# Performance work log

Measured on AMD Instinct MI355X. Metric: run time of the kernel, lower is better.

The kernel has to match this reference:

```python
import jax, jax.numpy as jnp
import numpy as np

N_TOKEN = 267735
D_EMBED = 1024
D_PROJ = 1024
CUTOFF_ENDS = [0, 20000, 40000, 200000, N_TOKEN]
DIV_VAL = 4
INIT_STD = 0.02


def setup_inputs() -> dict:
    key = jax.random.key(0)
    ks = jax.random.split(key, 9)
    inp = jax.random.randint(ks[0], (8, 4096), 0, N_TOKEN, dtype=jnp.int64)
    out = {"inp": inp}
    for i in range(4):
        l, r = CUTOFF_ENDS[i], CUTOFF_ENDS[i + 1]
        d_emb_i = D_EMBED // (DIV_VAL ** i)
        out[f"emb{i}"] = jax.random.normal(ks[1 + i], (r - l, d_emb_i), dtype=jnp.float32) * INIT_STD
        out[f"proj{i}"] = jax.random.normal(ks[5 + i], (d_emb_i, D_PROJ), dtype=jnp.float32) * INIT_STD
    return out


def reference(inp, emb0, emb1, emb2, emb3, proj0, proj1, proj2, proj3):
    embs = [emb0, emb1, emb2, emb3]
    projs = [proj0, proj1, proj2, proj3]
    flat = inp.reshape(-1)  # [N]
    out = jnp.zeros((flat.shape[0], D_PROJ), dtype=jnp.float32)
    for i in range(4):
        l, r = CUTOFF_ENDS[i], CUTOFF_ENDS[i + 1]
        mask = (flat >= l) & (flat < r)  # [N]
        idx = jnp.clip(flat - l, 0, r - l - 1)  # in-range even for out-of-bucket tokens
        e = embs[i][idx]                         # [N, d_emb_i] gather
        p = jnp.einsum('id,de->ie', e, projs[i])  # [N, D_PROJ]
        out = out + jnp.where(mask[:, None], p, 0.0)
    emb_scale = D_PROJ ** 0.5
    return (out * emb_scale).reshape(inp.shape + (D_PROJ,))
```

## Files before the change

### kernel.cpp

```cpp
#include <hip/hip_runtime.h>
#include <hip/hip_bf16.h>

#define N_TOK   32768
#define DPROJ   1024
#define SCALE   32.0f

typedef short bf16x8 __attribute__((ext_vector_type(8)));
typedef float f32x4  __attribute__((ext_vector_type(4)));

__device__ __forceinline__ short f2bf(float f) {
    unsigned u = __builtin_bit_cast(unsigned, f);
    unsigned r = (u + 0x7FFFu + ((u >> 16) & 1u)) >> 16;
    return (short)r;
}

__global__ void k_prep(const int* __restrict__ inp, int* __restrict__ cnt,
                       int* __restrict__ perm, int* __restrict__ rowidx,
                       const float* __restrict__ p0, const float* __restrict__ p1,
                       const float* __restrict__ p2, const float* __restrict__ p3,
                       short* __restrict__ t0, short* __restrict__ t1,
                       short* __restrict__ t2, short* __restrict__ t3)
{
    __shared__ float tile[128][17];

    if (blockIdx.x < 128) {
        int i = blockIdx.x * 256 + threadIdx.x;
        int t = inp[i];
        int b, l;
        if (t < 20000)       { b = 0; l = 0; }
        else if (t < 40000)  { b = 1; l = 20000; }
        else if (t < 200000) { b = 2; l = 40000; }
        else                 { b = 3; l = 200000; }

        unsigned long long m0 = __ballot(b == 0);
        unsigned long long m1 = __ballot(b == 1);
        unsigned long long m2 = __ballot(b == 2);
        unsigned long long m3 = __ballot(b == 3);

        int lane = threadIdx.x & 63;
        int mybase = 0;
        if (lane < 4) {
            unsigned long long mm = (lane == 0) ? m0 : (lane == 1) ? m1 : (lane == 2) ? m2 : m3;
            mybase = atomicAdd(&cnt[lane], __popcll(mm));
        }
        int base = __shfl(mybase, b);
        unsigned long long mine = (b == 0) ? m0 : (b == 1) ? m1 : (b == 2) ? m2 : m3;
        unsigned long long lt = (lane == 0) ? 0ull : (~0ull >> (64 - lane));
        int pos = base + __popcll(mine & lt);
        perm[b * N_TOK + pos]   = i;
        rowidx[b * N_TOK + pos] = t - l;
        return;
    }

    int bid = blockIdx.x - 128;
    const float* src; short* dst; int K; int rel;
    if (bid < 512)      { src = p0; dst = t0; K = 1024; rel = bid; }
    else if (bid < 640) { src = p1; dst = t1; K = 256;  rel = bid - 512; }
    else if (bid < 704) { src = p2; dst = t2; K = 64;   rel = bid - 640; }
    else                { src = p3; dst = t3; K = 16;   rel = bid - 704; }
    int ktiles = (K + 127) >> 7;
    int k0 = (rel % ktiles) * 128;
    int n0 = (rel / ktiles) * 16;
    int t = threadIdx.x;

    #pragma unroll
    for (int i = 0; i < 2; ++i) {
        int idx = t + i * 256;
        int k = idx >> 2;
        int nc = (idx & 3) * 4;
        if (k0 + k < K) {
            float4 v = *reinterpret_cast<const float4*>(src + (size_t)(k0 + k) * DPROJ + n0 + nc);
            tile[k][nc + 0] = v.x; tile[k][nc + 1] = v.y;
            tile[k][nc + 2] = v.z; tile[k][nc + 3] = v.w;
        }
    }
    __syncthreads();
    int n  = t >> 4;
    int kc = (t & 15) * 8;
    if (k0 + kc < K) {
        short s[8];
        #pragma unroll
        for (int j = 0; j < 8; ++j) s[j] = f2bf(tile[kc + j][n]);
        *reinterpret_cast<int4*>(dst + (size_t)(n0 + n) * K + k0 + kc) =
            *reinterpret_cast<const int4*>(s);
    }
}

__global__ __launch_bounds__(512, 4) void k_gemm(
    const float* __restrict__ e0, const float* __restrict__ e1,
    const float* __restrict__ e2, const float* __restrict__ e3,
    const short* __restrict__ t0, const short* __restrict__ t1,
    const short* __restrict__ t2, const short* __restrict__ t3,
    const int* __restrict__ cnt, const int* __restrict__ perm,
    const int* __restrict__ rowidx, float* __restrict__ out)
{
    __shared__ short As[64][40];
    __shared__ short Bs[256][40];

    const int hw     = blockIdx.y * 4 + blockIdx.x;
    const int ytile  = (hw >> 5) * 8 + (hw & 7);
    const int panel  = (hw >> 3) & 3;

    const int c0 = cnt[0], c1 = cnt[1], c2 = cnt[2], c3 = cnt[3];
    const int q0 = (c0 + 63) & ~63;
    const int q1 = q0 + ((c1 + 63) & ~63);
    const int q2 = q1 + ((c2 + 63) & ~63);
    const int q3 = q2 + ((c3 + 63) & ~63);
    const int p0 = ytile * 64;
    if (p0 >= q3) return;
    int b, M, m0, K; const float* emb; const short* bt;
    if (p0 < q0)      { b = 0; M = c0; m0 = p0;      K = 1024; emb = e0; bt = t0; }
    else if (p0 < q1) { b = 1; M = c1; m0 = p0 - q0; K = 256;  emb = e1; bt = t1; }
    else if (p0 < q2) { b = 2; M = c2; m0 = p0 - q1; K = 64;   emb = e2; bt = t2; }
    else              { b = 3; M = c3; m0 = p0 - q2; K = 16;   emb = e3; bt = t3; }
    if (m0 >= M) return;
    const int* pperm = perm   + b * N_TOK;
    const int* prow  = rowidx + b * N_TOK;

    const int tid  = threadIdx.x;
    const int lane = tid & 63;
    const int w    = tid >> 6;
    const int n0   = panel * 256;

    const int ar = tid >> 3;
    const int ac4 = (tid & 7) * 4;
    const bool avalid = (m0 + ar) < M;
    const int  arow   = avalid ? prow[m0 + ar] : 0;
    const float* aptr = emb + (size_t)arow * K;
    const int br = tid >> 1;
    const int bh = (tid & 1) * 16;

    f32x4 acc[4][2];
    #pragma unroll
    for (int mi = 0; mi < 4; ++mi)
        #pragma unroll
        for (int ni = 0; ni < 2; ++ni) acc[mi][ni] = (f32x4)0.0f;

    const int koff = (lane >> 4) * 8;
    const int fr   = lane & 15;

    float4 av;
    int4   bv0, bv1;
#define ISSUE_LOADS(K0)                                                        \
    {                                                                          \
        av = make_float4(0.f, 0.f, 0.f, 0.f);                                  \
        if (avalid && ((K0) + ac4) < K)                                        \
            av = *reinterpret_cast<const float4*>(aptr + (K0) + ac4);          \
        if (((K0) + bh) < K) {                                                 \
            const short* bp = bt + (size_t)(n0 + br) * K + (K0) + bh;          \
            bv0 = *reinterpret_cast<const int4*>(bp);                          \
            bv1 = *reinterpret_cast<const int4*>(bp + 8);                      \
        } else {                                                               \
            bv0 = make_int4(0, 0, 0, 0);                                       \
            bv1 = make_int4(0, 0, 0, 0);                                       \
        }                                                                      \
    }

    ISSUE_LOADS(0);
    for (int k0 = 0; k0 < K; k0 += 32) {
        __syncthreads();
        {
            short asv[4];
            asv[0] = f2bf(av.x); asv[1] = f2bf(av.y);
            asv[2] = f2bf(av.z); asv[3] = f2bf(av.w);
            *reinterpret_cast<int2*>(&As[ar][ac4]) = *reinterpret_cast<const int2*>(asv);
            *reinterpret_cast<int4*>(&Bs[br][bh])     = bv0;
            *reinterpret_cast<int4*>(&Bs[br][bh + 8]) = bv1;
        }
        if (k0 + 32 < K) ISSUE_LOADS(k0 + 32);
        __syncthreads();

        bf16x8 afr[4], bfr[2];
        #pragma unroll
        for (int mi = 0; mi < 4; ++mi)
            afr[mi] = *reinterpret_cast<const bf16x8*>(&As[mi * 16 + fr][koff]);
        #pragma unroll
        for (int ni = 0; ni < 2; ++ni)
            bfr[ni] = *reinterpret_cast<const bf16x8*>(&Bs[w * 32 + ni * 16 + fr][koff]);
        #pragma unroll
        for (int mi = 0; mi < 4; ++mi)
            #pragma unroll
            for (int ni = 0; ni < 2; ++ni)
                acc[mi][ni] = __builtin_amdgcn_mfma_f32_16x16x32_bf16(
                    afr[mi], bfr[ni], acc[mi][ni], 0, 0, 0);
    }
#undef ISSUE_LOADS

    const int colb = n0 + w * 32 + fr;
    const int rowg = (lane >> 4) * 4;
    #pragma unroll
    for (int mi = 0; mi < 4; ++mi) {
        #pragma unroll
        for (int j = 0; j < 4; ++j) {
            int m = m0 + mi * 16 + rowg + j;
            if (m < M) {
                size_t r = (size_t)pperm[m] * DPROJ + colb;
                out[r]      = acc[mi][0][j] * SCALE;
                out[r + 16] = acc[mi][1][j] * SCALE;
            }
        }
    }
}

__global__ void k_naive(const int* __restrict__ inp,
                        const float* __restrict__ emb0, const float* __restrict__ emb1,
                        const float* __restrict__ emb2, const float* __restrict__ emb3,
                        const float* __restrict__ proj0, const float* __restrict__ proj1,
                        const float* __restrict__ proj2, const float* __restrict__ proj3,
                        float* __restrict__ out)
{
    __shared__ float e[1024];
    int t = inp[blockIdx.x];
    const float* emb; const float* proj; int K, l;
    if (t < 20000)       { emb = emb0; proj = proj0; K = 1024; l = 0; }
    else if (t < 40000)  { emb = emb1; proj = proj1; K = 256;  l = 20000; }
    else if (t < 200000) { emb = emb2; proj = proj2; K = 64;   l = 40000; }
    else                 { emb = emb3; proj = proj3; K = 16;   l = 200000; }
    int tid = threadIdx.x;
    for (int k = tid; k < K; k += 256) e[k] = emb[(size_t)(t - l) * K + k];
    __syncthreads();
    float acc[4] = {0.f, 0.f, 0.f, 0.f};
    for (int k = 0; k < K; ++k) {
        float ek = e[k];
        #pragma unroll
        for (int c = 0; c < 4; ++c)
            acc[c] = fmaf(ek, proj[(size_t)k * DPROJ + tid + 256 * c], acc[c]);
    }
    #pragma unroll
    for (int c = 0; c < 4; ++c)
        out[(size_t)blockIdx.x * DPROJ + tid + 256 * c] = acc[c] * SCALE;
}

extern "C" void kernel_launch(void* const* d_in, const int* in_sizes, int n_in,
                              void* d_out, int out_size, void* d_ws, size_t ws_size,
                              hipStream_t stream) {
    const int*   inp   = (const int*)d_in[0];
    const float* emb0  = (const float*)d_in[1];
    const float* proj0 = (const float*)d_in[2];
    const float* emb1  = (const float*)d_in[3];
    const float* proj1 = (const float*)d_in[4];
    const float* emb2  = (const float*)d_in[5];
    const float* proj2 = (const float*)d_in[6];
    const float* emb3  = (const float*)d_in[7];
    const float* proj3 = (const float*)d_in[8];
    float* out = (float*)d_out;

    const size_t off_cnt  = 0;
    const size_t off_perm = 256;
    const size_t off_row  = off_perm + 4ull * N_TOK * 4;
    const size_t off_t0   = off_row  + 4ull * N_TOK * 4;
    const size_t off_t1   = off_t0 + 1024ull * 1024 * 2;
    const size_t off_t2   = off_t1 + 1024ull * 256 * 2;
    const size_t off_t3   = off_t2 + 1024ull * 64 * 2;
    const size_t needed   = off_t3 + 1024ull * 16 * 2;

    if (d_ws == nullptr || ws_size < needed) {
        k_naive<<<N_TOK, 256, 0, stream>>>(inp, emb0, emb1, emb2, emb3,
                                           proj0, proj1, proj2, proj3, out);
        return;
    }

    char* ws = (char*)d_ws;
    int*   cnt    = (int*)(ws + off_cnt);
    int*   perm   = (int*)(ws + off_perm);
    int*   rowidx = (int*)(ws + off_row);
    short* t0     = (short*)(ws + off_t0);
    short* t1     = (short*)(ws + off_t1);
    short* t2     = (short*)(ws + off_t2);
    short* t3     = (short*)(ws + off_t3);

    hipMemsetAsync(cnt, 0, 16, stream);
    k_prep<<<896, 256, 0, stream>>>(inp, cnt, perm, rowidx,
                                    proj0, proj1, proj2, proj3, t0, t1, t2, t3);

    dim3 grid(4, 520);
    k_gemm<<<grid, 512, 0, stream>>>(emb0, emb1, emb2, emb3,
                                     t0, t1, t2, t3,
                                     cnt, perm, rowidx, out);
}
```

Baseline: 54.39 us.

## Shrink GEMM N-tile to 128 with 2x4 warp grid and prefetch perm rows

The gather-GEMM block tile changes from 64x256 to 64x128, doubling the grid to 8 panels per row tile and remapping the swizzle. Warps are arranged 2x4 over M and N, so each wave computes a 32x32 sub-tile, and launch bounds now request 8 blocks per CU. Output permutation indices are loaded into registers before the main loop instead of during the epilogue. The goal is more concurrent blocks and lower LDS use per block, in exchange for re-gathering and re-converting the A rows twice as often across panels.

```diff
diff --git a/kernel.cpp b/kernel.cpp
--- a/kernel.cpp
+++ b/kernel.cpp
@@ -86,7 +86,7 @@
     }
 }
 
-__global__ __launch_bounds__(512, 4) void k_gemm(
+__global__ __launch_bounds__(512, 8) void k_gemm(
     const float* __restrict__ e0, const float* __restrict__ e1,
     const float* __restrict__ e2, const float* __restrict__ e3,
     const short* __restrict__ t0, const short* __restrict__ t1,
@@ -95,11 +95,11 @@
     const int* __restrict__ rowidx, float* __restrict__ out)
 {
     __shared__ short As[64][40];
-    __shared__ short Bs[256][40];
-
-    const int hw     = blockIdx.y * 4 + blockIdx.x;
-    const int ytile  = (hw >> 5) * 8 + (hw & 7);
-    const int panel  = (hw >> 3) & 3;
+    __shared__ short Bs[128][40];
+
+    const int hw    = blockIdx.y * 8 + blockIdx.x;
+    const int ytile = (hw >> 6) * 8 + (hw & 7);
+    const int panel = (hw >> 3) & 7;
 
     const int c0 = cnt[0], c1 = cnt[1], c2 = cnt[2], c3 = cnt[3];
     const int q0 = (c0 + 63) & ~63;
@@ -120,40 +120,48 @@
     const int tid  = threadIdx.x;
     const int lane = tid & 63;
     const int w    = tid >> 6;
-    const int n0   = panel * 256;
-
-    const int ar = tid >> 3;
-    const int ac4 = (tid & 7) * 4;
+    const int wr   = w >> 2;
+    const int wc   = w & 3;
+    const int n0   = panel * 128;
+
+    const int ar  = tid >> 3;
+    const int ac  = (tid & 7) * 4;
     const bool avalid = (m0 + ar) < M;
     const int  arow   = avalid ? prow[m0 + ar] : 0;
     const float* aptr = emb + (size_t)arow * K;
-    const int br = tid >> 1;
-    const int bh = (tid & 1) * 16;
-
-    f32x4 acc[4][2];
-    #pragma unroll
-    for (int mi = 0; mi < 4; ++mi)
-        #pragma unroll
-        for (int ni = 0; ni < 2; ++ni) acc[mi][ni] = (f32x4)0.0f;
+    const int br = tid >> 2;
+    const int bq = (tid & 3) * 8;
 
     const int koff = (lane >> 4) * 8;
     const int fr   = lane & 15;
+    const int rowg = (lane >> 4) * 4;
+
+    int pr[2][4];
+    #pragma unroll
+    for (int mi = 0; mi < 2; ++mi)
+        #pragma unroll
+        for (int j = 0; j < 4; ++j) {
+            int m = m0 + wr * 32 + mi * 16 + rowg + j;
+            pr[mi][j] = (m < M) ? pperm[m] : 0;
+        }
+
+    f32x4 acc[2][2];
+    #pragma unroll
+    for (int mi = 0; mi < 2; ++mi)
+        #pragma unroll
+        for (int ni = 0; ni < 2; ++ni) acc[mi][ni] = (f32x4)0.0f;
 
     float4 av;
-    int4   bv0, bv1;
+    int4   bv;
 #define ISSUE_LOADS(K0)                                                        \
     {                                                                          \
         av = make_float4(0.f, 0.f, 0.f, 0.f);                                  \
-        if (avalid && ((K0) + ac4) < K)                                        \
-            av = *reinterpret_cast<const float4*>(aptr + (K0) + ac4);          \
-        if (((K0) + bh) < K) {                                                 \
-            const short* bp = bt + (size_t)(n0 + br) * K + (K0) + bh;          \
-            bv0 = *reinterpret_cast<const int4*>(bp);                          \
-            bv1 = *reinterpret_cast<const int4*>(bp + 8);                      \
-        } else {                                                               \
-            bv0 = make_int4(0, 0, 0, 0);                                       \
-            bv1 = make_int4(0, 0, 0, 0);                                       \
-        }                                                                      \
+        if (avalid && ((K0) + ac) < K)                                         \
+            av = *reinterpret_cast<const float4*>(aptr + (K0) + ac);           \
+        if (((K0) + bq) < K)                                                   \
+            bv = *reinterpret_cast<const int4*>(                               \
+                bt + (size_t)(n0 + br) * K + (K0) + bq);                       \
+        else bv = make_int4(0, 0, 0, 0);                                       \
     }
 
     ISSUE_LOADS(0);
@@ -163,22 +171,21 @@
             short asv[4];
             asv[0] = f2bf(av.x); asv[1] = f2bf(av.y);
             asv[2] = f2bf(av.z); asv[3] = f2bf(av.w);
-            *reinterpret_cast<int2*>(&As[ar][ac4]) = *reinterpret_cast<const int2*>(asv);
-            *reinterpret_cast<int4*>(&Bs[br][bh])     = bv0;
-            *reinterpret_cast<int4*>(&Bs[br][bh + 8]) = bv1;
+            *reinterpret_cast<int2*>(&As[ar][ac]) = *reinterpret_cast<const int2*>(asv);
+            *reinterpret_cast<int4*>(&Bs[br][bq]) = bv;
         }
         if (k0 + 32 < K) ISSUE_LOADS(k0 + 32);
         __syncthreads();
 
-        bf16x8 afr[4], bfr[2];
-        #pragma unroll
-        for (int mi = 0; mi < 4; ++mi)
-            afr[mi] = *reinterpret_cast<const bf16x8*>(&As[mi * 16 + fr][koff]);
+        bf16x8 afr[2], bfr[2];
+        #pragma unroll
+        for (int mi = 0; mi < 2; ++mi)
+            afr[mi] = *reinterpret_cast<const bf16x8*>(&As[wr * 32 + mi * 16 + fr][koff]);
         #pragma unroll
         for (int ni = 0; ni < 2; ++ni)
-            bfr[ni] = *reinterpret_cast<const bf16x8*>(&Bs[w * 32 + ni * 16 + fr][koff]);
-        #pragma unroll
-        for (int mi = 0; mi < 4; ++mi)
+            bfr[ni] = *reinterpret_cast<const bf16x8*>(&Bs[wc * 32 + ni * 16 + fr][koff]);
+        #pragma unroll
+        for (int mi = 0; mi < 2; ++mi)
             #pragma unroll
             for (int ni = 0; ni < 2; ++ni)
                 acc[mi][ni] = __builtin_amdgcn_mfma_f32_16x16x32_bf16(
@@ -186,15 +193,14 @@
     }
 #undef ISSUE_LOADS
 
-    const int colb = n0 + w * 32 + fr;
-    const int rowg = (lane >> 4) * 4;
-    #pragma unroll
-    for (int mi = 0; mi < 4; ++mi) {
+    const int colb = n0 + wc * 32 + fr;
+    #pragma unroll
+    for (int mi = 0; mi < 2; ++mi) {
         #pragma unroll
         for (int j = 0; j < 4; ++j) {
-            int m = m0 + mi * 16 + rowg + j;
+            int m = m0 + wr * 32 + mi * 16 + rowg + j;
             if (m < M) {
-                size_t r = (size_t)pperm[m] * DPROJ + colb;
+                size_t r = (size_t)pr[mi][j] * DPROJ + colb;
                 out[r]      = acc[mi][0][j] * SCALE;
                 out[r + 16] = acc[mi][1][j] * SCALE;
             }
@@ -273,7 +279,7 @@
     k_prep<<<896, 256, 0, stream>>>(inp, cnt, perm, rowidx,
                                     proj0, proj1, proj2, proj3, t0, t1, t2, t3);
 
-    dim3 grid(4, 520);
+    dim3 grid(8, 520);
     k_gemm<<<grid, 512, 0, stream>>>(emb0, emb1, emb2, emb3,
                                      t0, t1, t2, t3,
                                      cnt, perm, rowidx, out);
```

New measurement: 59.27 us. +9.0%, slower.

## Double-buffer LDS and specialize GEMM body per bucket K via templates

Applied to the files above, without the earlier changes.

The bucketed GEMM kernel moves into a template on K so each bucket's loop trip count and bounds checks are fixed at compile time. Shared memory is now double-buffered, with global loads issued two steps ahead. This lets the MFMA work on one buffer overlap the LDS writes for the next and drops one barrier per step. Output permutation indices are also loaded up front. In exchange, LDS use doubles and register pressure rises, which may lower occupancy under the 512x4 launch bounds.

```diff
diff --git a/kernel.cpp b/kernel.cpp
--- a/kernel.cpp
+++ b/kernel.cpp
@@ -86,6 +86,145 @@
     }
 }
 
+template<int K>
+__device__ __forceinline__ void gemm_body(
+    const float* __restrict__ emb, const short* __restrict__ bt,
+    int M, int m0, const int* __restrict__ pperm, const int* __restrict__ prow,
+    int n0, float* __restrict__ out,
+    short (&As)[2][64][40], short (&Bs)[2][256][40])
+{
+    constexpr int NSTEP = (K + 31) / 32;
+
+    const int tid  = threadIdx.x;
+    const int lane = tid & 63;
+    const int w    = tid >> 6;
+
+    const int ar = tid >> 3;
+    const int ac = (tid & 7) * 4;
+    const int br = tid >> 1;
+    const int bh = (tid & 1) * 16;
+    const bool avalid = (m0 + ar) < M;
+    const int  arow   = avalid ? prow[m0 + ar] : 0;
+    const float* aptr = emb + (size_t)arow * K;
+
+    const int koff = (lane >> 4) * 8;
+    const int fr   = lane & 15;
+    const int rowg = (lane >> 4) * 4;
+
+    int pr[4][4];
+    #pragma unroll
+    for (int mi = 0; mi < 4; ++mi)
+        #pragma unroll
+        for (int j = 0; j < 4; ++j) {
+            int m = m0 + mi * 16 + rowg + j;
+            pr[mi][j] = (m < M) ? pperm[m] : 0;
+        }
+
+    f32x4 acc[4][2];
+    #pragma unroll
+    for (int mi = 0; mi < 4; ++mi)
+        #pragma unroll
+        for (int ni = 0; ni < 2; ++ni) acc[mi][ni] = (f32x4)0.0f;
+
+    float4 av0, av1;
+    int4   b00, b01, b10, b11;
+
+#define LOADK0(KS)                                                             \
+    {                                                                          \
+        av0 = make_float4(0.f, 0.f, 0.f, 0.f);                                 \
+        if (avalid && (K >= 32 || ac < K))                                     \
+            av0 = *reinterpret_cast<const float4*>(aptr + (KS) * 32 + ac);     \
+        if (K >= 32 || bh < K) {                                               \
+            const short* bp = bt + (size_t)(n0 + br) * K + (KS) * 32 + bh;     \
+            b00 = *reinterpret_cast<const int4*>(bp);                          \
+            b01 = *reinterpret_cast<const int4*>(bp + 8);                      \
+        } else { b00 = make_int4(0,0,0,0); b01 = make_int4(0,0,0,0); }         \
+    }
+#define LOADK1(KS)                                                             \
+    {                                                                          \
+        av1 = make_float4(0.f, 0.f, 0.f, 0.f);                                 \
+        if (avalid && (K >= 32 || ac < K))                                     \
+            av1 = *reinterpret_cast<const float4*>(aptr + (KS) * 32 + ac);     \
+        if (K >= 32 || bh < K) {                                               \
+            const short* bp = bt + (size_t)(n0 + br) * K + (KS) * 32 + bh;     \
+            b10 = *reinterpret_cast<const int4*>(bp);                          \
+            b11 = *reinterpret_cast<const int4*>(bp + 8);                      \
+        } else { b10 = make_int4(0,0,0,0); b11 = make_int4(0,0,0,0); }         \
+    }
+#define WRITEK(CUR, AV, B0, B1)                                                \
+    {                                                                          \
+        short asv[4];                                                          \
+        asv[0] = f2bf((AV).x); asv[1] = f2bf((AV).y);                          \
+        asv[2] = f2bf((AV).z); asv[3] = f2bf((AV).w);                          \
+        *reinterpret_cast<int2*>(&As[CUR][ar][ac]) =                           \
+            *reinterpret_cast<const int2*>(asv);                               \
+        *reinterpret_cast<int4*>(&Bs[CUR][br][bh])     = (B0);                 \
+        *reinterpret_cast<int4*>(&Bs[CUR][br][bh + 8]) = (B1);                 \
+    }
+#define MFMAK(CUR)                                                             \
+    {                                                                          \
+        bf16x8 afr[4], bfr[2];                                                 \
+        _Pragma("unroll")                                                      \
+        for (int mi = 0; mi < 4; ++mi)                                         \
+            afr[mi] = *reinterpret_cast<const bf16x8*>(                        \
+                &As[CUR][mi * 16 + fr][koff]);                                 \
+        _Pragma("unroll")                                                      \
+        for (int ni = 0; ni < 2; ++ni)                                         \
+            bfr[ni] = *reinterpret_cast<const bf16x8*>(                        \
+                &Bs[CUR][w * 32 + ni * 16 + fr][koff]);                        \
+        _Pragma("unroll")                                                      \
+        for (int mi = 0; mi < 4; ++mi)                                         \
+            _Pragma("unroll")                                                  \
+            for (int ni = 0; ni < 2; ++ni)                                     \
+                acc[mi][ni] = __builtin_amdgcn_mfma_f32_16x16x32_bf16(         \
+                    afr[mi], bfr[ni], acc[mi][ni], 0, 0, 0);                   \
+    }
+
+    if constexpr (NSTEP == 1) {
+        LOADK0(0);
+        WRITEK(0, av0, b00, b01);
+        __syncthreads();
+        MFMAK(0);
+    } else {
+        LOADK0(0);
+        WRITEK(0, av0, b00, b01);
+        LOADK0(1);
+        if constexpr (NSTEP > 2) LOADK1(2);
+        __syncthreads();
+
+        for (int k = 0; k < NSTEP; k += 2) {
+            if (k + 1 < NSTEP) WRITEK(1, av0, b00, b01);
+            if (k + 3 < NSTEP) LOADK0(k + 3);
+            MFMAK(0);
+            __syncthreads();
+            if (k + 1 < NSTEP) {
+                if (k + 2 < NSTEP) WRITEK(0, av1, b10, b11);
+                if (k + 4 < NSTEP) LOADK1(k + 4);
+                MFMAK(1);
+                __syncthreads();
+            }
+        }
+    }
+#undef LOADK0
+#undef LOADK1
+#undef WRITEK
+#undef MFMAK
+
+    const int colb = n0 + w * 32 + fr;
+    #pragma unroll
+    for (int mi = 0; mi < 4; ++mi) {
+        #pragma unroll
+        for (int j = 0; j < 4; ++j) {
+            int m = m0 + mi * 16 + rowg + j;
+            if (m < M) {
+                size_t r = (size_t)pr[mi][j] * DPROJ + colb;
+                out[r]      = acc[mi][0][j] * SCALE;
+                out[r + 16] = acc[mi][1][j] * SCALE;
+            }
+        }
+    }
+}
+
 __global__ __launch_bounds__(512, 4) void k_gemm(
     const float* __restrict__ e0, const float* __restrict__ e1,
     const float* __restrict__ e2, const float* __restrict__ e3,
@@ -94,12 +233,12 @@
     const int* __restrict__ cnt, const int* __restrict__ perm,
     const int* __restrict__ rowidx, float* __restrict__ out)
 {
-    __shared__ short As[64][40];
-    __shared__ short Bs[256][40];
-
-    const int hw     = blockIdx.y * 4 + blockIdx.x;
-    const int ytile  = (hw >> 5) * 8 + (hw & 7);
-    const int panel  = (hw >> 3) & 3;
+    __shared__ short As[2][64][40];
+    __shared__ short Bs[2][256][40];
+
+    const int hw    = blockIdx.y * 4 + blockIdx.x;
+    const int ytile = (hw >> 5) * 8 + (hw & 7);
+    const int panel = (hw >> 3) & 3;
 
     const int c0 = cnt[0], c1 = cnt[1], c2 = cnt[2], c3 = cnt[3];
     const int q0 = (c0 + 63) & ~63;
@@ -108,97 +247,23 @@
     const int q3 = q2 + ((c3 + 63) & ~63);
     const int p0 = ytile * 64;
     if (p0 >= q3) return;
-    int b, M, m0, K; const float* emb; const short* bt;
-    if (p0 < q0)      { b = 0; M = c0; m0 = p0;      K = 1024; emb = e0; bt = t0; }
-    else if (p0 < q1) { b = 1; M = c1; m0 = p0 - q0; K = 256;  emb = e1; bt = t1; }
-    else if (p0 < q2) { b = 2; M = c2; m0 = p0 - q1; K = 64;   emb = e2; bt = t2; }
-    else              { b = 3; M = c3; m0 = p0 - q2; K = 16;   emb = e3; bt = t3; }
-    if (m0 >= M) return;
-    const int* pperm = perm   + b * N_TOK;
-    const int* prow  = rowidx + b * N_TOK;
-
-    const int tid  = threadIdx.x;
-    const int lane = tid & 63;
-    const int w    = tid >> 6;
-    const int n0   = panel * 256;
-
-    const int ar = tid >> 3;
-    const int ac4 = (tid & 7) * 4;
-    const bool avalid = (m0 + ar) < M;
-    const int  arow   = avalid ? prow[m0 + ar] : 0;
-    const float* aptr = emb + (size_t)arow * K;
-    const int br = tid >> 1;
-    const int bh = (tid & 1) * 16;
-
-    f32x4 acc[4][2];
-    #pragma unroll
-    for (int mi = 0; mi < 4; ++mi)
-        #pragma unroll
-        for (int ni = 0; ni < 2; ++ni) acc[mi][ni] = (f32x4)0.0f;
-
-    const int koff = (lane >> 4) * 8;
-    const int fr   = lane & 15;
-
-    float4 av;
-    int4   bv0, bv1;
-#define ISSUE_LOADS(K0)                                                        \
-    {                                                                          \
-        av = make_float4(0.f, 0.f, 0.f, 0.f);                                  \
-        if (avalid && ((K0) + ac4) < K)                                        \
-            av = *reinterpret_cast<const float4*>(aptr + (K0) + ac4);          \
-        if (((K0) + bh) < K) {                                                 \
-            const short* bp = bt + (size_t)(n0 + br) * K + (K0) + bh;          \
-            bv0 = *reinterpret_cast<const int4*>(bp);                          \
-            bv1 = *reinterpret_cast<const int4*>(bp + 8);                      \
-        } else {                                                               \
-            bv0 = make_int4(0, 0, 0, 0);                                       \
-            bv1 = make_int4(0, 0, 0, 0);                                       \
-        }                                                                      \
-    }
-
-    ISSUE_LOADS(0);
-    for (int k0 = 0; k0 < K; k0 += 32) {
-        __syncthreads();
-        {
-            short asv[4];
-            asv[0] = f2bf(av.x); asv[1] = f2bf(av.y);
-            asv[2] = f2bf(av.z); asv[3] = f2bf(av.w);
-            *reinterpret_cast<int2*>(&As[ar][ac4]) = *reinterpret_cast<const int2*>(asv);
-            *reinterpret_cast<int4*>(&Bs[br][bh])     = bv0;
-            *reinterpret_cast<int4*>(&Bs[br][bh + 8]) = bv1;
-        }
-        if (k0 + 32 < K) ISSUE_LOADS(k0 + 32);
-        __syncthreads();
-
-        bf16x8 afr[4], bfr[2];
-        #pragma unroll
-        for (int mi = 0; mi < 4; ++mi)
-            afr[mi] = *reinterpret_cast<const bf16x8*>(&As[mi * 16 + fr][koff]);
-        #pragma unroll
-        for (int ni = 0; ni < 2; ++ni)
-            bfr[ni] = *reinterpret_cast<const bf16x8*>(&Bs[w * 32 + ni * 16 + fr][koff]);
-        #pragma unroll
-        for (int mi = 0; mi < 4; ++mi)
-            #pragma unroll
-            for (int ni = 0; ni < 2; ++ni)
-                acc[mi][ni] = __builtin_amdgcn_mfma_f32_16x16x32_bf16(
-                    afr[mi], bfr[ni], acc[mi][ni], 0, 0, 0);
-    }
-#undef ISSUE_LOADS
-
-    const int colb = n0 + w * 32 + fr;
-    const int rowg = (lane >> 4) * 4;
-    #pragma unroll
-    for (int mi = 0; mi < 4; ++mi) {
-        #pragma unroll
-        for (int j = 0; j < 4; ++j) {
-            int m = m0 + mi * 16 + rowg + j;
-            if (m < M) {
-                size_t r = (size_t)pperm[m] * DPROJ + colb;
-                out[r]      = acc[mi][0][j] * SCALE;
-                out[r + 16] = acc[mi][1][j] * SCALE;
-            }
-        }
+    const int n0 = panel * 256;
+
+    if (p0 < q0) {
+        if (p0 >= c0) return;
+        gemm_body<1024>(e0, t0, c0, p0, perm, rowidx, n0, out, As, Bs);
+    } else if (p0 < q1) {
+        int m0 = p0 - q0;
+        if (m0 >= c1) return;
+        gemm_body<256>(e1, t1, c1, m0, perm + N_TOK, rowidx + N_TOK, n0, out, As, Bs);
+    } else if (p0 < q2) {
+        int m0 = p0 - q1;
+        if (m0 >= c2) return;
+        gemm_body<64>(e2, t2, c2, m0, perm + 2 * N_TOK, rowidx + 2 * N_TOK, n0, out, As, Bs);
+    } else {
+        int m0 = p0 - q2;
+        if (m0 >= c3) return;
+        gemm_body<16>(e3, t3, c3, m0, perm + 3 * N_TOK, rowidx + 3 * N_TOK, n0, out, As, Bs);
     }
 }
 
```

Measured after the change: 58.94 us. 1.08x slower.

## Specialize GEMM per bucket K and fold scale into projection

Applied to the files above, without the earlier changes.

The grouped GEMM is split into templated bodies with compile-time K. Deep buckets (K=1024, 256) keep the pipelined LDS loop but lose the bounds checks. Short buckets (K=64, 16) load the B fragments straight from global into registers and run a single-stage MFMA without a loop. The output scale is folded into the bf16 transposed projection, and the permutation indices are prefetched before the main loop. The risks are extra code size and register pressure, plus a slightly different rounding, because the scale is applied before the bf16 conversion.

```diff
diff --git a/kernel.cpp b/kernel.cpp
--- a/kernel.cpp
+++ b/kernel.cpp
@@ -80,9 +80,214 @@
     if (k0 + kc < K) {
         short s[8];
         #pragma unroll
-        for (int j = 0; j < 8; ++j) s[j] = f2bf(tile[kc + j][n]);
+        for (int j = 0; j < 8; ++j) s[j] = f2bf(tile[kc + j][n] * 32.0f);
         *reinterpret_cast<int4*>(dst + (size_t)(n0 + n) * K + k0 + kc) =
             *reinterpret_cast<const int4*>(s);
+    }
+}
+
+template<int K>
+__device__ __forceinline__ void body_deep(
+    const float* __restrict__ emb, const short* __restrict__ bt,
+    int M, int m0, const int* __restrict__ pperm, const int* __restrict__ prow,
+    int n0, float* __restrict__ out,
+    short (&As)[64][40], short (&Bs)[256][40])
+{
+    const int tid  = threadIdx.x;
+    const int lane = tid & 63;
+    const int w    = tid >> 6;
+    const int ar   = tid >> 3;
+    const int ac   = (tid & 7) * 4;
+    const int br   = tid >> 1;
+    const int bh   = (tid & 1) * 16;
+    const bool avalid = (m0 + ar) < M;
+    const int  arow   = avalid ? prow[m0 + ar] : 0;
+    const float* aptr = emb + (size_t)arow * K;
+
+    const int koff = (lane >> 4) * 8;
+    const int fr   = lane & 15;
+    const int rowg = (lane >> 4) * 4;
+
+    int pr[4][4];
+    #pragma unroll
+    for (int mi = 0; mi < 4; ++mi)
+        #pragma unroll
+        for (int j = 0; j < 4; ++j) {
+            int m = m0 + mi * 16 + rowg + j;
+            pr[mi][j] = (m < M) ? pperm[m] : 0;
+        }
+
+    f32x4 acc[4][2];
+    #pragma unroll
+    for (int mi = 0; mi < 4; ++mi)
+        #pragma unroll
+        for (int ni = 0; ni < 2; ++ni) acc[mi][ni] = (f32x4)0.0f;
+
+    float4 av;
+    int4   bv0, bv1;
+#define ISSUE_LOADS(K0)                                                        \
+    {                                                                          \
+        av = avalid ? *reinterpret_cast<const float4*>(aptr + (K0) + ac)       \
+                    : make_float4(0.f, 0.f, 0.f, 0.f);                         \
+        const short* bp = bt + (size_t)(n0 + br) * K + (K0) + bh;              \
+        bv0 = *reinterpret_cast<const int4*>(bp);                              \
+        bv1 = *reinterpret_cast<const int4*>(bp + 8);                          \
+    }
+
+    ISSUE_LOADS(0);
+    for (int k0 = 0; k0 < K; k0 += 32) {
+        __syncthreads();
+        {
+            short asv[4];
+            asv[0] = f2bf(av.x); asv[1] = f2bf(av.y);
+            asv[2] = f2bf(av.z); asv[3] = f2bf(av.w);
+            *reinterpret_cast<int2*>(&As[ar][ac]) = *reinterpret_cast<const int2*>(asv);
+            *reinterpret_cast<int4*>(&Bs[br][bh])     = bv0;
+            *reinterpret_cast<int4*>(&Bs[br][bh + 8]) = bv1;
+        }
+        if (k0 + 32 < K) ISSUE_LOADS(k0 + 32);
+        __syncthreads();
+
+        bf16x8 afr[4], bfr[2];
+        #pragma unroll
+        for (int mi = 0; mi < 4; ++mi)
+            afr[mi] = *reinterpret_cast<const bf16x8*>(&As[mi * 16 + fr][koff]);
+        #pragma unroll
+        for (int ni = 0; ni < 2; ++ni)
+            bfr[ni] = *reinterpret_cast<const bf16x8*>(&Bs[w * 32 + ni * 16 + fr][koff]);
+        #pragma unroll
+        for (int mi = 0; mi < 4; ++mi)
+            #pragma unroll
+            for (int ni = 0; ni < 2; ++ni)
+                acc[mi][ni] = __builtin_amdgcn_mfma_f32_16x16x32_bf16(
+                    afr[mi], bfr[ni], acc[mi][ni], 0, 0, 0);
+    }
+#undef ISSUE_LOADS
+
+    const int colb = n0 + w * 32 + fr;
+    #pragma unroll
+    for (int mi = 0; mi < 4; ++mi) {
+        #pragma unroll
+        for (int j = 0; j < 4; ++j) {
+            int m = m0 + mi * 16 + rowg + j;
+            if (m < M) {
+                size_t r = (size_t)pr[mi][j] * DPROJ + colb;
+                out[r]      = acc[mi][0][j];
+                out[r + 16] = acc[mi][1][j];
+            }
+        }
+    }
+}
+
+template<int K>
+__device__ __forceinline__ void body_short(
+    const float* __restrict__ emb, const short* __restrict__ bt,
+    int M, int m0, const int* __restrict__ pperm, const int* __restrict__ prow,
+    int n0, float* __restrict__ out,
+    short (&As)[64][40], short (&Bs)[256][40])
+{
+    constexpr int NKF = (K == 64) ? 2 : 1;
+
+    const int tid  = threadIdx.x;
+    const int lane = tid & 63;
+    const int w    = tid >> 6;
+    const int koff = (lane >> 4) * 8;
+    const int fr   = lane & 15;
+    const int rowg = (lane >> 4) * 4;
+
+    int pr[4][4];
+    #pragma unroll
+    for (int mi = 0; mi < 4; ++mi)
+        #pragma unroll
+        for (int j = 0; j < 4; ++j) {
+            int m = m0 + mi * 16 + rowg + j;
+            pr[mi][j] = (m < M) ? pperm[m] : 0;
+        }
+
+    const short* btw = bt + (size_t)(n0 + w * 32 + fr) * K;
+    bf16x8 bfr[2][NKF];
+    #pragma unroll
+    for (int ni = 0; ni < 2; ++ni)
+        #pragma unroll
+        for (int kf = 0; kf < NKF; ++kf) {
+            if (K == 16 && koff >= 16)
+                bfr[ni][kf] = (bf16x8)0;
+            else
+                bfr[ni][kf] = *reinterpret_cast<const bf16x8*>(
+                    btw + (size_t)ni * 16 * K + kf * 32 + koff);
+        }
+
+    f32x4 acc[4][2];
+    #pragma unroll
+    for (int mi = 0; mi < 4; ++mi)
+        #pragma unroll
+        for (int ni = 0; ni < 2; ++ni) acc[mi][ni] = (f32x4)0.0f;
+
+    if constexpr (K == 64) {
+        short (*As2)[72] = reinterpret_cast<short(*)[72]>(&Bs[0][0]);
+        const int row = tid >> 3;
+        const int c   = (tid & 7) * 8;
+        const bool av = (m0 + row) < M;
+        const int  ar = av ? prow[m0 + row] : 0;
+        const float* ap = emb + (size_t)ar * 64 + c;
+        float4 x = *reinterpret_cast<const float4*>(ap);
+        float4 y = *reinterpret_cast<const float4*>(ap + 4);
+        short s[8];
+        s[0] = f2bf(x.x); s[1] = f2bf(x.y); s[2] = f2bf(x.z); s[3] = f2bf(x.w);
+        s[4] = f2bf(y.x); s[5] = f2bf(y.y); s[6] = f2bf(y.z); s[7] = f2bf(y.w);
+        *reinterpret_cast<int4*>(&As2[row][c]) = *reinterpret_cast<const int4*>(s);
+        __syncthreads();
+
+        #pragma unroll
+        for (int mi = 0; mi < 4; ++mi) {
+            bf16x8 afr0 = *reinterpret_cast<const bf16x8*>(&As2[mi * 16 + fr][koff]);
+            bf16x8 afr1 = *reinterpret_cast<const bf16x8*>(&As2[mi * 16 + fr][32 + koff]);
+            #pragma unroll
+            for (int ni = 0; ni < 2; ++ni) {
+                acc[mi][ni] = __builtin_amdgcn_mfma_f32_16x16x32_bf16(
+                    afr0, bfr[ni][0], acc[mi][ni], 0, 0, 0);
+                acc[mi][ni] = __builtin_amdgcn_mfma_f32_16x16x32_bf16(
+                    afr1, bfr[ni][1], acc[mi][ni], 0, 0, 0);
+            }
+        }
+    } else {
+        const int row = tid >> 3;
+        const int c   = (tid & 7) * 4;
+        if (c < 16) {
+            const bool av = (m0 + row) < M;
+            const int  ar = av ? prow[m0 + row] : 0;
+            float4 x = *reinterpret_cast<const float4*>(emb + (size_t)ar * 16 + c);
+            short s[4];
+            s[0] = f2bf(x.x); s[1] = f2bf(x.y); s[2] = f2bf(x.z); s[3] = f2bf(x.w);
+            *reinterpret_cast<int2*>(&As[row][c]) = *reinterpret_cast<const int2*>(s);
+        } else {
+            int z[2] = {0, 0};
+            *reinterpret_cast<int2*>(&As[row][c]) = *reinterpret_cast<const int2*>(z);
+        }
+        __syncthreads();
+
+        #pragma unroll
+        for (int mi = 0; mi < 4; ++mi) {
+            bf16x8 afr = *reinterpret_cast<const bf16x8*>(&As[mi * 16 + fr][koff]);
+            #pragma unroll
+            for (int ni = 0; ni < 2; ++ni)
+                acc[mi][ni] = __builtin_amdgcn_mfma_f32_16x16x32_bf16(
+                    afr, bfr[ni][0], acc[mi][ni], 0, 0, 0);
+        }
+    }
+
+    const int colb = n0 + w * 32 + fr;
+    #pragma unroll
+    for (int mi = 0; mi < 4; ++mi) {
+        #pragma unroll
+        for (int j = 0; j < 4; ++j) {
+            int m = m0 + mi * 16 + rowg + j;
+            if (m < M) {
+                size_t r = (size_t)pr[mi][j] * DPROJ + colb;
+                out[r]      = acc[mi][0][j];
+                out[r + 16] = acc[mi][1][j];
+            }
+        }
     }
 }
 
@@ -97,9 +302,9 @@
     __shared__ short As[64][40];
     __shared__ short Bs[256][40];
 
-    const int hw     = blockIdx.y * 4 + blockIdx.x;
-    const int ytile  = (hw >> 5) * 8 + (hw & 7);
-    const int panel  = (hw >> 3) & 3;
+    const int hw    = blockIdx.y * 4 + blockIdx.x;
+    const int ytile = (hw >> 5) * 8 + (hw & 7);
+    const int panel = (hw >> 3) & 3;
 
     const int c0 = cnt[0], c1 = cnt[1], c2 = cnt[2], c3 = cnt[3];
     const int q0 = (c0 + 63) & ~63;
@@ -108,97 +313,19 @@
     const int q3 = q2 + ((c3 + 63) & ~63);
     const int p0 = ytile * 64;
     if (p0 >= q3) return;
-    int b, M, m0, K; const float* emb; const short* bt;
-    if (p0 < q0)      { b = 0; M = c0; m0 = p0;      K = 1024; emb = e0; bt = t0; }
-    else if (p0 < q1) { b = 1; M = c1; m0 = p0 - q0; K = 256;  emb = e1; bt = t1; }
-    else if (p0 < q2) { b = 2; M = c2; m0 = p0 - q1; K = 64;   emb = e2; bt = t2; }
-    else              { b = 3; M = c3; m0 = p0 - q2; K = 16;   emb = e3; bt = t3; }
-    if (m0 >= M) return;
-    const int* pperm = perm   + b * N_TOK;
-    const int* prow  = rowidx + b * N_TOK;
-
-    const int tid  = threadIdx.x;
-    const int lane = tid & 63;
-    const int w    = tid >> 6;
-    const int n0   = panel * 256;
-
-    const int ar = tid >> 3;
-    const int ac4 = (tid & 7) * 4;
-    const bool avalid = (m0 + ar) < M;
-    const int  arow   = avalid ? prow[m0 + ar] : 0;
-    const float* aptr = emb + (size_t)arow * K;
-    const int br = tid >> 1;
-    const int bh = (tid & 1) * 16;
-
-    f32x4 acc[4][2];
-    #pragma unroll
-    for (int mi = 0; mi < 4; ++mi)
-        #pragma unroll
-        for (int ni = 0; ni < 2; ++ni) acc[mi][ni] = (f32x4)0.0f;
-
-    const int koff = (lane >> 4) * 8;
-    const int fr   = lane & 15;
-
-    float4 av;
-    int4   bv0, bv1;
-#define ISSUE_LOADS(K0)                                                        \
-    {                                                                          \
-        av = make_float4(0.f, 0.f, 0.f, 0.f);                                  \
-        if (avalid && ((K0) + ac4) < K)                                        \
-            av = *reinterpret_cast<const float4*>(aptr + (K0) + ac4);          \
-        if (((K0) + bh) < K) {                                                 \
-            const short* bp = bt + (size_t)(n0 + br) * K + (K0) + bh;          \
-            bv0 = *reinterpret_cast<const int4*>(bp);                          \
-            bv1 = *reinterpret_cast<const int4*>(bp + 8);                      \
-        } else {                                                               \
-            bv0 = make_int4(0, 0, 0, 0);                                       \
-            bv1 = make_int4(0, 0, 0, 0);                                       \
-        }                                                                      \
-    }
-
-    ISSUE_LOADS(0);
-    for (int k0 = 0; k0 < K; k0 += 32) {
-        __syncthreads();
-        {
-            short asv[4];
-            asv[0] = f2bf(av.x); asv[1] = f2bf(av.y);
-            asv[2] = f2bf(av.z); asv[3] = f2bf(av.w);
-            *reinterpret_cast<int2*>(&As[ar][ac4]) = *reinterpret_cast<const int2*>(asv);
-            *reinterpret_cast<int4*>(&Bs[br][bh])     = bv0;
-            *reinterpret_cast<int4*>(&Bs[br][bh + 8]) = bv1;
-        }
-        if (k0 + 32 < K) ISSUE_LOADS(k0 + 32);
-        __syncthreads();
-
-        bf16x8 afr[4], bfr[2];
-        #pragma unroll
-        for (int mi = 0; mi < 4; ++mi)
-            afr[mi] = *reinterpret_cast<const bf16x8*>(&As[mi * 16 + fr][koff]);
-        #pragma unroll
-        for (int ni = 0; ni < 2; ++ni)
-            bfr[ni] = *reinterpret_cast<const bf16x8*>(&Bs[w * 32 + ni * 16 + fr][koff]);
-        #pragma unroll
-        for (int mi = 0; mi < 4; ++mi)
-            #pragma unroll
-            for (int ni = 0; ni < 2; ++ni)
-                acc[mi][ni] = __builtin_amdgcn_mfma_f32_16x16x32_bf16(
-                    afr[mi], bfr[ni], acc[mi][ni], 0, 0, 0);
-    }
-#undef ISSUE_LOADS
-
-    const int colb = n0 + w * 32 + fr;
-    const int rowg = (lane >> 4) * 4;
-    #pragma unroll
-    for (int mi = 0; mi < 4; ++mi) {
-        #pragma unroll
-        for (int j = 0; j < 4; ++j) {
-            int m = m0 + mi * 16 + rowg + j;
-            if (m < M) {
-                size_t r = (size_t)pperm[m] * DPROJ + colb;
-                out[r]      = acc[mi][0][j] * SCALE;
-                out[r + 16] = acc[mi][1][j] * SCALE;
-            }
-        }
+    const int n0 = panel * 256;
+
+    if (p0 < q0) {
+        body_deep<1024>(e0, t0, c0, p0, perm, rowidx, n0, out, As, Bs);
+    } else if (p0 < q1) {
+        body_deep<256>(e1, t1, c1, p0 - q0, perm + N_TOK, rowidx + N_TOK,
+                       n0, out, As, Bs);
+    } else if (p0 < q2) {
+        body_short<64>(e2, t2, c2, p0 - q1, perm + 2 * N_TOK,
+                       rowidx + 2 * N_TOK, n0, out, As, Bs);
+    } else {
+        body_short<16>(e3, t3, c3, p0 - q2, perm + 3 * N_TOK,
+                       rowidx + 3 * N_TOK, n0, out, As, Bs);
     }
 }
 
```

New measurement: 59.60 us. +9.6%, slower.
